# Performance work log

Hardware: AMD Instinct MI355X
Metric: run time of the kernel (lower is better)

Reference implementation:

```python
import jax, jax.numpy as jnp
import numpy as np

HIDDEN, FFN, N_EXPERTS, TOP_K = 1024, 4096, 8, 2


def setup_inputs() -> dict:
    key = jax.random.key(0)
    ks = jax.random.split(key, 8)
    s_h = 1.0 / np.sqrt(HIDDEN)
    s_f = 1.0 / np.sqrt(FFN)
    return {
        "x": jax.random.normal(ks[0], (1, 1024, HIDDEN), dtype=jnp.float32),
        "gate_w": jax.random.normal(ks[1], (N_EXPERTS, HIDDEN), dtype=jnp.float32) * s_h,
        "gate_b": jnp.zeros((N_EXPERTS,), dtype=jnp.float32),
        "w1": jax.random.normal(ks[2], (N_EXPERTS, HIDDEN, FFN), dtype=jnp.float32) * s_h,
        "b1": jnp.zeros((N_EXPERTS, FFN), dtype=jnp.float32),
        "w2": jax.random.normal(ks[3], (N_EXPERTS, FFN, HIDDEN), dtype=jnp.float32) * s_f,
        "b2": jnp.zeros((N_EXPERTS, HIDDEN), dtype=jnp.float32),
    }


def reference(x, gate_w, gate_b, w1, b1, w2, b2):
    B, S, H = x.shape
    x_flat = x.reshape(-1, H)  # (T, H)
    # Router: top-k gating with softmax over selected logits
    logits = x_flat @ gate_w.T + gate_b  # (T, E)
    top_w, sel = jax.lax.top_k(logits, TOP_K)  # (T, K)
    rw = jax.nn.softmax(top_w, axis=-1)  # (T, K)
    # combine[t, e] = router weight of expert e for token t (0 if not selected)
    combine = jnp.sum(jax.nn.one_hot(sel, N_EXPERTS, dtype=x.dtype) * rw[..., None], axis=1)  # (T, E)
    # Dense all-expert FFN, combined with routing weights (zero weight => zero contribution,
    # identical math to the masked gather/scatter loop in the torch module)
    h = jax.nn.gelu(jnp.einsum('th,ehf->tef', x_flat, w1) + b1, approximate=False)  # (T, E, F)
    y = jnp.einsum('tef,efh->teh', h, w2) + b2  # (T, E, H)
    out = jnp.einsum('te,teh->th', combine, y)  # (T, H)
    return out.reshape(B, S, H)
```

## Files before the change

kernel.cpp:

```cpp
#include <hip/hip_runtime.h>


typedef __bf16 bf16;
typedef __bf16 bf16x8 __attribute__((ext_vector_type(8)));
typedef float floatx4 __attribute__((ext_vector_type(4)));

#define T_TOK 1024
#define HID 1024
#define FFN 4096
#define NEXP 8
#define BM 128
#define BN 128
#define BK 32

#define GLOAD16(g, l) __builtin_amdgcn_global_load_lds( \
    (const __attribute__((address_space(1))) void*)(g), \
    (__attribute__((address_space(3))) void*)(l), 16, 0, 0)

__device__ __forceinline__ void wconv_body(const float* __restrict__ w,
                                           bf16* __restrict__ wt, int bid, int tid,
                                           int K, int N, int lgN, int lgKC) {
  int gid = bid * 256 + tid;
  int n = gid & (N - 1);
  int kc = (gid >> lgN) & ((K >> 5) - 1);
  int e = gid >> (lgN + lgKC);
  const float* src = w + ((size_t)e * K + (size_t)kc * 32) * N + n;
  bf16* dst = wt + ((size_t)e * N + n) * (size_t)K + kc * 32;
  float v[32];
#pragma unroll
  for (int j = 0; j < 32; j++) v[j] = src[(size_t)j * N];
  bf16x8 pk[4];
#pragma unroll
  for (int q = 0; q < 4; q++)
#pragma unroll
    for (int i = 0; i < 8; i++) pk[q][i] = (bf16)v[q * 8 + i];
#pragma unroll
  for (int q = 0; q < 4; q++) *(bf16x8*)(dst + q * 8) = pk[q];
}

__device__ __forceinline__ void xconv_body(const float* __restrict__ x,
                                           bf16* __restrict__ xb, int bid, int tid) {
  int i = bid * 256 + tid;
  float4 a = ((const float4*)x)[i * 2];
  float4 b = ((const float4*)x)[i * 2 + 1];
  bf16 t[8] = {(bf16)a.x, (bf16)a.y, (bf16)a.z, (bf16)a.w,
               (bf16)b.x, (bf16)b.y, (bf16)b.z, (bf16)b.w};
  *(bf16x8*)&xb[(size_t)i * 8] = *(bf16x8*)t;
}

__device__ __forceinline__ void router_body(const float* __restrict__ x,
                                            const float* __restrict__ gw,
                                            const float* __restrict__ gb,
                                            int* __restrict__ cnt, int* __restrict__ elist,
                                            float* __restrict__ ewt, int bid, int tid) {
  int wave = tid >> 6;
  int lane = tid & 63;
  int t = bid * 4 + wave;
  const float* xr = x + (size_t)t * HID;
  float xv[16];
#pragma unroll
  for (int j = 0; j < 16; j++) xv[j] = xr[lane + 64 * j];
  float logits[NEXP];
#pragma unroll
  for (int e = 0; e < NEXP; e++) {
    const float* g = gw + (size_t)e * HID;
    float s = 0.f;
#pragma unroll
    for (int j = 0; j < 16; j++) s += xv[j] * g[lane + 64 * j];
#pragma unroll
    for (int off = 32; off; off >>= 1) s += __shfl_xor(s, off, 64);
    logits[e] = s + gb[e];
  }
  int i0 = 0; float l0 = logits[0];
#pragma unroll
  for (int e = 1; e < NEXP; e++) if (logits[e] > l0) { l0 = logits[e]; i0 = e; }
  int i1 = -1; float l1 = -3.0e38f;
#pragma unroll
  for (int e = 0; e < NEXP; e++) if (e != i0 && logits[e] > l1) { l1 = logits[e]; i1 = e; }
  if (lane == 0) {
    float w0 = 1.f / (1.f + expf(l1 - l0));
    float w1 = 1.f - w0;
    int p0 = atomicAdd(cnt + i0, 1);
    elist[i0 * T_TOK + p0] = t * 2 + 0; ewt[i0 * T_TOK + p0] = w0;
    int p1 = atomicAdd(cnt + i1, 1);
    elist[i1 * T_TOK + p1] = t * 2 + 1; ewt[i1 * T_TOK + p1] = w1;
  }
}

__global__ __launch_bounds__(256)
void fusedB_k(const float* __restrict__ x, bf16* __restrict__ xb,
              const float* __restrict__ gw, const float* __restrict__ gb,
              int* __restrict__ cnt, int* __restrict__ elist, float* __restrict__ ewt,
              const float* __restrict__ w1, bf16* __restrict__ w1t) {
  int bid = blockIdx.x;
  int tid = threadIdx.x;
  if (bid < 4096) { wconv_body(w1, w1t, bid, tid, HID, FFN, 12, 5); return; }
  bid -= 4096;
  if (bid < 512) { xconv_body(x, xb, bid, tid); return; }
  router_body(x, gw, gb, cnt, elist, ewt, bid - 512, tid);
}

__global__ __launch_bounds__(256)
void wconv_k(const float* __restrict__ w, bf16* __restrict__ wt,
             int K, int N, int lgN, int lgKC) {
  wconv_body(w, wt, blockIdx.x, threadIdx.x, K, N, lgN, lgKC);
}

__global__ __launch_bounds__(256)
void gemm1f_k(int nconv, const float* __restrict__ w2, bf16* __restrict__ w2t,
              const bf16* __restrict__ xb, const bf16* __restrict__ w1t,
              const float* __restrict__ b1, const int* __restrict__ cnt,
              const int* __restrict__ elist, bf16* __restrict__ hbuf) {
  int tid = threadIdx.x;
  int bid = blockIdx.x;
  if (bid < nconv) { wconv_body(w2, w2t, bid, tid, FFN, HID, 10, 7); return; }
  int g = bid - nconv;
  int e = g >> 8;
  int m0 = ((g >> 5) & 7) * BM;
  int n0 = (g & 31) * BN;
  int c = cnt[e];
  if (m0 >= c) return;

  __shared__ __align__(16) bf16 As[BM][BK];
  __shared__ __align__(16) bf16 Bs[BN][BK];

  int l = tid & 63, w = tid >> 6;
  int rr = w * 32 + (l >> 2);
  int cb = (l & 3) * 8;
  int ga0 = m0 + rr;      if (ga0 >= c) ga0 = c - 1;
  int ga1 = m0 + rr + 16; if (ga1 >= c) ga1 = c - 1;
  const bf16* aS0 = xb + (size_t)(elist[e * T_TOK + ga0] >> 1) * HID + cb;
  const bf16* aS1 = xb + (size_t)(elist[e * T_TOK + ga1] >> 1) * HID + cb;
  const bf16* w1te = w1t + (size_t)e * FFN * HID;
  const bf16* bS0 = w1te + (size_t)(n0 + rr) * HID + cb;
  const bf16* bS1 = w1te + (size_t)(n0 + rr + 16) * HID + cb;
  bf16* ldA0 = &As[w * 32][0];
  bf16* ldA1 = &As[w * 32 + 16][0];
  bf16* ldB0 = &Bs[w * 32][0];
  bf16* ldB1 = &Bs[w * 32 + 16][0];

  floatx4 acc[4][4] = {};
  int fm = l & 15, quad = l >> 4, wm = (w & 1) * 64, wn = (w >> 1) * 64;

  for (int t = 0; t < HID / BK; t++) {
    __syncthreads();
    GLOAD16(aS0, ldA0); GLOAD16(aS1, ldA1);
    GLOAD16(bS0, ldB0); GLOAD16(bS1, ldB1);
    aS0 += BK; aS1 += BK; bS0 += BK; bS1 += BK;
    __syncthreads();
    bf16x8 af[4], bfr[4];
#pragma unroll
    for (int i = 0; i < 4; i++) af[i] = *(const bf16x8*)&As[wm + i * 16 + fm][quad * 8];
#pragma unroll
    for (int j = 0; j < 4; j++) bfr[j] = *(const bf16x8*)&Bs[wn + j * 16 + fm][quad * 8];
#pragma unroll
    for (int i = 0; i < 4; i++)
#pragma unroll
      for (int j = 0; j < 4; j++)
        acc[i][j] = __builtin_amdgcn_mfma_f32_16x16x32_bf16(af[i], bfr[j], acc[i][j], 0, 0, 0);
  }

  const float* b1e = b1 + (size_t)e * FFN;
#pragma unroll
  for (int i = 0; i < 4; i++) {
    int rb = m0 + wm + i * 16 + quad * 4;
#pragma unroll
    for (int j = 0; j < 4; j++) {
      int col = n0 + wn + j * 16 + fm;
      float bias = b1e[col];
#pragma unroll
      for (int r = 0; r < 4; r++) {
        int row = rb + r;
        if (row < c) {
          int slot = elist[e * T_TOK + row];
          float v = acc[i][j][r] + bias;
          float gl = 0.5f * v * (1.f + erff(v * 0.70710678118654752f));
          hbuf[(size_t)slot * FFN + col] = (bf16)gl;
        }
      }
    }
  }
}

__global__ __launch_bounds__(256)
void gemm2_k(const bf16* __restrict__ hbuf, const bf16* __restrict__ w2t,
             const float* __restrict__ b2, const int* __restrict__ cnt,
             const int* __restrict__ elist, const float* __restrict__ ewt,
             float* __restrict__ out) {
  int e = blockIdx.z & 7;
  int ks = blockIdx.z >> 3;
  int c = cnt[e];
  int m0 = blockIdx.y * BM;
  if (m0 >= c) return;
  int n0 = blockIdx.x * BN;
  int kbeg = ks * (FFN / 4);

  __shared__ __align__(16) bf16 As[BM][BK];
  __shared__ __align__(16) bf16 Bs[BN][BK];

  int tid = threadIdx.x;
  int l = tid & 63, w = tid >> 6;
  int rr = w * 32 + (l >> 2);
  int cb = (l & 3) * 8;
  int ga0 = m0 + rr;      if (ga0 >= c) ga0 = c - 1;
  int ga1 = m0 + rr + 16; if (ga1 >= c) ga1 = c - 1;
  const bf16* aS0 = hbuf + (size_t)elist[e * T_TOK + ga0] * FFN + kbeg + cb;
  const bf16* aS1 = hbuf + (size_t)elist[e * T_TOK + ga1] * FFN + kbeg + cb;
  const bf16* w2te = w2t + (size_t)e * HID * FFN;
  const bf16* bS0 = w2te + (size_t)(n0 + rr) * FFN + kbeg + cb;
  const bf16* bS1 = w2te + (size_t)(n0 + rr + 16) * FFN + kbeg + cb;
  bf16* ldA0 = &As[w * 32][0];
  bf16* ldA1 = &As[w * 32 + 16][0];
  bf16* ldB0 = &Bs[w * 32][0];
  bf16* ldB1 = &Bs[w * 32 + 16][0];

  floatx4 acc[4][4] = {};
  int fm = l & 15, quad = l >> 4, wm = (w & 1) * 64, wn = (w >> 1) * 64;

  const int NT = (FFN / 4) / BK;
  for (int t = 0; t < NT; t++) {
    __syncthreads();
    GLOAD16(aS0, ldA0); GLOAD16(aS1, ldA1);
    GLOAD16(bS0, ldB0); GLOAD16(bS1, ldB1);
    aS0 += BK; aS1 += BK; bS0 += BK; bS1 += BK;
    __syncthreads();
    bf16x8 af[4], bfr[4];
#pragma unroll
    for (int i = 0; i < 4; i++) af[i] = *(const bf16x8*)&As[wm + i * 16 + fm][quad * 8];
#pragma unroll
    for (int j = 0; j < 4; j++) bfr[j] = *(const bf16x8*)&Bs[wn + j * 16 + fm][quad * 8];
#pragma unroll
    for (int i = 0; i < 4; i++)
#pragma unroll
      for (int j = 0; j < 4; j++)
        acc[i][j] = __builtin_amdgcn_mfma_f32_16x16x32_bf16(af[i], bfr[j], acc[i][j], 0, 0, 0);
  }

  const float* b2e = b2 + (size_t)e * HID;
#pragma unroll
  for (int i = 0; i < 4; i++) {
    int rb = m0 + wm + i * 16 + quad * 4;
#pragma unroll
    for (int j = 0; j < 4; j++) {
      int col = n0 + wn + j * 16 + fm;
      float bias = (ks == 0) ? b2e[col] : 0.f;
#pragma unroll
      for (int r = 0; r < 4; r++) {
        int row = rb + r;
        if (row < c) {
          int slot = elist[e * T_TOK + row];
          float wgt = ewt[e * T_TOK + row];
          atomicAdd(&out[(size_t)(slot >> 1) * HID + col], wgt * (acc[i][j][r] + bias));
        }
      }
    }
  }
}

extern "C" void kernel_launch(void* const* d_in, const int* in_sizes, int n_in,
                              void* d_out, int out_size, void* d_ws, size_t ws_size,
                              hipStream_t stream) {
  const float* x  = (const float*)d_in[0];
  const float* gw = (const float*)d_in[1];
  const float* gb = (const float*)d_in[2];
  const float* w1 = (const float*)d_in[3];
  const float* b1 = (const float*)d_in[4];
  const float* w2 = (const float*)d_in[5];
  const float* b2 = (const float*)d_in[6];
  float* out = (float*)d_out;

  char* ws = (char*)d_ws;
  int*   cnt   = (int*)ws;
  int*   elist = (int*)(ws + 1024);
  float* ewt   = (float*)(ws + 1024 + 32768);
  bf16*  xb    = (bf16*)(ws + (1 << 16));
  bf16*  hbuf  = (bf16*)(ws + ((size_t)4 << 20));
  bf16*  w1T   = (bf16*)(ws + ((size_t)21 << 20));
  bool par = ws_size >= ((size_t)157 << 20);
  bf16*  w2T   = par ? (bf16*)(ws + ((size_t)89 << 20))
                     : w1T;

  hipMemsetAsync(cnt, 0, 32, stream);
  hipMemsetAsync(out, 0, out_size, stream);
  fusedB_k<<<4864, 256, 0, stream>>>(x, xb, gw, gb, cnt, elist, ewt, w1, w1T);
  if (par) {
    gemm1f_k<<<4096 + 2048, 256, 0, stream>>>(4096, w2, w2T, xb, w1T, b1, cnt, elist, hbuf);
  } else {
    gemm1f_k<<<2048, 256, 0, stream>>>(0, w2, w2T, xb, w1T, b1, cnt, elist, hbuf);
    wconv_k<<<4096, 256, 0, stream>>>(w2, w2T, FFN, HID, 10, 7);
  }
  gemm2_k<<<dim3(HID / BN, T_TOK / BM, NEXP * 4), 256, 0, stream>>>(hbuf, w2T, b2, cnt, elist, ewt, out);
}
```

Baseline: 524.6 us.

## Shrink GEMM M-tile to 64 and deepen K-step to 64 in both expert GEMMs

Both grouped GEMMs now use 64-row by 128-column tiles with a 64-wide K step, stored as two 32-wide LDS halves. Each warp covers all 64 rows and a 32-column strip. In the fused first kernel the GEMM blocks now come first and the w2 conversion blocks come last. Smaller M tiles waste less work on partially filled expert tiles and give more blocks, and the deeper K step halves the number of barriers. The cost is lower reuse per block, since more blocks reload the same weight columns.

```diff
diff --git a/kernel.cpp b/kernel.cpp
--- a/kernel.cpp
+++ b/kernel.cpp
@@ -9,9 +9,9 @@
 #define HID 1024
 #define FFN 4096
 #define NEXP 8
-#define BM 128
+#define BM 64
 #define BN 128
-#define BK 32
+#define BK 64
 
 #define GLOAD16(g, l) __builtin_amdgcn_global_load_lds( \
     (const __attribute__((address_space(1))) void*)(g), \
@@ -107,65 +107,71 @@
 }
 
 __global__ __launch_bounds__(256)
-void gemm1f_k(int nconv, const float* __restrict__ w2, bf16* __restrict__ w2t,
+void gemm1f_k(int ngemm, const float* __restrict__ w2, bf16* __restrict__ w2t,
               const bf16* __restrict__ xb, const bf16* __restrict__ w1t,
               const float* __restrict__ b1, const int* __restrict__ cnt,
               const int* __restrict__ elist, bf16* __restrict__ hbuf) {
   int tid = threadIdx.x;
   int bid = blockIdx.x;
-  if (bid < nconv) { wconv_body(w2, w2t, bid, tid, FFN, HID, 10, 7); return; }
-  int g = bid - nconv;
-  int e = g >> 8;
-  int m0 = ((g >> 5) & 7) * BM;
-  int n0 = (g & 31) * BN;
+  if (bid >= ngemm) { wconv_body(w2, w2t, bid - ngemm, tid, FFN, HID, 10, 7); return; }
+  int e = bid >> 9;
+  int m0 = ((bid >> 5) & 15) * BM;
+  int n0 = (bid & 31) * BN;
   int c = cnt[e];
   if (m0 >= c) return;
 
-  __shared__ __align__(16) bf16 As[BM][BK];
-  __shared__ __align__(16) bf16 Bs[BN][BK];
+  __shared__ __align__(16) bf16 As[2][BM][32];
+  __shared__ __align__(16) bf16 Bs[2][BN][32];
 
   int l = tid & 63, w = tid >> 6;
-  int rr = w * 32 + (l >> 2);
-  int cb = (l & 3) * 8;
-  int ga0 = m0 + rr;      if (ga0 >= c) ga0 = c - 1;
-  int ga1 = m0 + rr + 16; if (ga1 >= c) ga1 = c - 1;
-  const bf16* aS0 = xb + (size_t)(elist[e * T_TOK + ga0] >> 1) * HID + cb;
-  const bf16* aS1 = xb + (size_t)(elist[e * T_TOK + ga1] >> 1) * HID + cb;
+  int l4 = l >> 2;
+  int k8 = (l & 3) * 8;
+  int gra = m0 + w * 16 + l4; if (gra >= c) gra = c - 1;
+  const bf16* ap = xb + (size_t)(elist[e * T_TOK + gra] >> 1) * HID + k8;
   const bf16* w1te = w1t + (size_t)e * FFN * HID;
-  const bf16* bS0 = w1te + (size_t)(n0 + rr) * HID + cb;
-  const bf16* bS1 = w1te + (size_t)(n0 + rr + 16) * HID + cb;
-  bf16* ldA0 = &As[w * 32][0];
-  bf16* ldA1 = &As[w * 32 + 16][0];
-  bf16* ldB0 = &Bs[w * 32][0];
-  bf16* ldB1 = &Bs[w * 32 + 16][0];
-
-  floatx4 acc[4][4] = {};
-  int fm = l & 15, quad = l >> 4, wm = (w & 1) * 64, wn = (w >> 1) * 64;
+  const bf16* bp0 = w1te + (size_t)(n0 + (2 * w) * 16 + l4) * HID + k8;
+  const bf16* bp1 = w1te + (size_t)(n0 + (2 * w + 1) * 16 + l4) * HID + k8;
+  bf16* ldA0 = &As[0][w * 16][0];
+  bf16* ldA1 = &As[1][w * 16][0];
+  bf16* ldB00 = &Bs[0][(2 * w) * 16][0];
+  bf16* ldB01 = &Bs[1][(2 * w) * 16][0];
+  bf16* ldB10 = &Bs[0][(2 * w + 1) * 16][0];
+  bf16* ldB11 = &Bs[1][(2 * w + 1) * 16][0];
+
+  floatx4 acc[4][2] = {};
+  int fm = l & 15, quad = l >> 4;
+  int wn = w * 32;
 
   for (int t = 0; t < HID / BK; t++) {
     __syncthreads();
-    GLOAD16(aS0, ldA0); GLOAD16(aS1, ldA1);
-    GLOAD16(bS0, ldB0); GLOAD16(bS1, ldB1);
-    aS0 += BK; aS1 += BK; bS0 += BK; bS1 += BK;
+    GLOAD16(ap, ldA0);       GLOAD16(ap + 32, ldA1);
+    GLOAD16(bp0, ldB00);     GLOAD16(bp0 + 32, ldB01);
+    GLOAD16(bp1, ldB10);     GLOAD16(bp1 + 32, ldB11);
+    ap += BK; bp0 += BK; bp1 += BK;
     __syncthreads();
-    bf16x8 af[4], bfr[4];
-#pragma unroll
-    for (int i = 0; i < 4; i++) af[i] = *(const bf16x8*)&As[wm + i * 16 + fm][quad * 8];
-#pragma unroll
-    for (int j = 0; j < 4; j++) bfr[j] = *(const bf16x8*)&Bs[wn + j * 16 + fm][quad * 8];
-#pragma unroll
-    for (int i = 0; i < 4; i++)
-#pragma unroll
-      for (int j = 0; j < 4; j++)
-        acc[i][j] = __builtin_amdgcn_mfma_f32_16x16x32_bf16(af[i], bfr[j], acc[i][j], 0, 0, 0);
+    bf16x8 af[2][4], bfr[2][2];
+#pragma unroll
+    for (int kk = 0; kk < 2; kk++) {
+#pragma unroll
+      for (int i = 0; i < 4; i++) af[kk][i] = *(const bf16x8*)&As[kk][i * 16 + fm][quad * 8];
+#pragma unroll
+      for (int j = 0; j < 2; j++) bfr[kk][j] = *(const bf16x8*)&Bs[kk][wn + j * 16 + fm][quad * 8];
+    }
+#pragma unroll
+    for (int kk = 0; kk < 2; kk++)
+#pragma unroll
+      for (int i = 0; i < 4; i++)
+#pragma unroll
+        for (int j = 0; j < 2; j++)
+          acc[i][j] = __builtin_amdgcn_mfma_f32_16x16x32_bf16(af[kk][i], bfr[kk][j], acc[i][j], 0, 0, 0);
   }
 
   const float* b1e = b1 + (size_t)e * FFN;
 #pragma unroll
   for (int i = 0; i < 4; i++) {
-    int rb = m0 + wm + i * 16 + quad * 4;
-#pragma unroll
-    for (int j = 0; j < 4; j++) {
+    int rb = m0 + i * 16 + quad * 4;
+#pragma unroll
+    for (int j = 0; j < 2; j++) {
       int col = n0 + wn + j * 16 + fm;
       float bias = b1e[col];
 #pragma unroll
@@ -195,53 +201,60 @@
   int n0 = blockIdx.x * BN;
   int kbeg = ks * (FFN / 4);
 
-  __shared__ __align__(16) bf16 As[BM][BK];
-  __shared__ __align__(16) bf16 Bs[BN][BK];
+  __shared__ __align__(16) bf16 As[2][BM][32];
+  __shared__ __align__(16) bf16 Bs[2][BN][32];
 
   int tid = threadIdx.x;
   int l = tid & 63, w = tid >> 6;
-  int rr = w * 32 + (l >> 2);
-  int cb = (l & 3) * 8;
-  int ga0 = m0 + rr;      if (ga0 >= c) ga0 = c - 1;
-  int ga1 = m0 + rr + 16; if (ga1 >= c) ga1 = c - 1;
-  const bf16* aS0 = hbuf + (size_t)elist[e * T_TOK + ga0] * FFN + kbeg + cb;
-  const bf16* aS1 = hbuf + (size_t)elist[e * T_TOK + ga1] * FFN + kbeg + cb;
+  int l4 = l >> 2;
+  int k8 = (l & 3) * 8;
+  int gra = m0 + w * 16 + l4; if (gra >= c) gra = c - 1;
+  const bf16* ap = hbuf + (size_t)elist[e * T_TOK + gra] * FFN + kbeg + k8;
   const bf16* w2te = w2t + (size_t)e * HID * FFN;
-  const bf16* bS0 = w2te + (size_t)(n0 + rr) * FFN + kbeg + cb;
-  const bf16* bS1 = w2te + (size_t)(n0 + rr + 16) * FFN + kbeg + cb;
-  bf16* ldA0 = &As[w * 32][0];
-  bf16* ldA1 = &As[w * 32 + 16][0];
-  bf16* ldB0 = &Bs[w * 32][0];
-  bf16* ldB1 = &Bs[w * 32 + 16][0];
-
-  floatx4 acc[4][4] = {};
-  int fm = l & 15, quad = l >> 4, wm = (w & 1) * 64, wn = (w >> 1) * 64;
+  const bf16* bp0 = w2te + (size_t)(n0 + (2 * w) * 16 + l4) * FFN + kbeg + k8;
+  const bf16* bp1 = w2te + (size_t)(n0 + (2 * w + 1) * 16 + l4) * FFN + kbeg + k8;
+  bf16* ldA0 = &As[0][w * 16][0];
+  bf16* ldA1 = &As[1][w * 16][0];
+  bf16* ldB00 = &Bs[0][(2 * w) * 16][0];
+  bf16* ldB01 = &Bs[1][(2 * w) * 16][0];
+  bf16* ldB10 = &Bs[0][(2 * w + 1) * 16][0];
+  bf16* ldB11 = &Bs[1][(2 * w + 1) * 16][0];
+
+  floatx4 acc[4][2] = {};
+  int fm = l & 15, quad = l >> 4;
+  int wn = w * 32;
 
   const int NT = (FFN / 4) / BK;
   for (int t = 0; t < NT; t++) {
     __syncthreads();
-    GLOAD16(aS0, ldA0); GLOAD16(aS1, ldA1);
-    GLOAD16(bS0, ldB0); GLOAD16(bS1, ldB1);
-    aS0 += BK; aS1 += BK; bS0 += BK; bS1 += BK;
+    GLOAD16(ap, ldA0);       GLOAD16(ap + 32, ldA1);
+    GLOAD16(bp0, ldB00);     GLOAD16(bp0 + 32, ldB01);
+    GLOAD16(bp1, ldB10);     GLOAD16(bp1 + 32, ldB11);
+    ap += BK; bp0 += BK; bp1 += BK;
     __syncthreads();
-    bf16x8 af[4], bfr[4];
-#pragma unroll
-    for (int i = 0; i < 4; i++) af[i] = *(const bf16x8*)&As[wm + i * 16 + fm][quad * 8];
-#pragma unroll
-    for (int j = 0; j < 4; j++) bfr[j] = *(const bf16x8*)&Bs[wn + j * 16 + fm][quad * 8];
-#pragma unroll
-    for (int i = 0; i < 4; i++)
-#pragma unroll
-      for (int j = 0; j < 4; j++)
-        acc[i][j] = __builtin_amdgcn_mfma_f32_16x16x32_bf16(af[i], bfr[j], acc[i][j], 0, 0, 0);
+    bf16x8 af[2][4], bfr[2][2];
+#pragma unroll
+    for (int kk = 0; kk < 2; kk++) {
+#pragma unroll
+      for (int i = 0; i < 4; i++) af[kk][i] = *(const bf16x8*)&As[kk][i * 16 + fm][quad * 8];
+#pragma unroll
+      for (int j = 0; j < 2; j++) bfr[kk][j] = *(const bf16x8*)&Bs[kk][wn + j * 16 + fm][quad * 8];
+    }
+#pragma unroll
+    for (int kk = 0; kk < 2; kk++)
+#pragma unroll
+      for (int i = 0; i < 4; i++)
+#pragma unroll
+        for (int j = 0; j < 2; j++)
+          acc[i][j] = __builtin_amdgcn_mfma_f32_16x16x32_bf16(af[kk][i], bfr[kk][j], acc[i][j], 0, 0, 0);
   }
 
   const float* b2e = b2 + (size_t)e * HID;
 #pragma unroll
   for (int i = 0; i < 4; i++) {
-    int rb = m0 + wm + i * 16 + quad * 4;
-#pragma unroll
-    for (int j = 0; j < 4; j++) {
+    int rb = m0 + i * 16 + quad * 4;
+#pragma unroll
+    for (int j = 0; j < 2; j++) {
       int col = n0 + wn + j * 16 + fm;
       float bias = (ks == 0) ? b2e[col] : 0.f;
 #pragma unroll
@@ -284,9 +297,9 @@
   hipMemsetAsync(out, 0, out_size, stream);
   fusedB_k<<<4864, 256, 0, stream>>>(x, xb, gw, gb, cnt, elist, ewt, w1, w1T);
   if (par) {
-    gemm1f_k<<<4096 + 2048, 256, 0, stream>>>(4096, w2, w2T, xb, w1T, b1, cnt, elist, hbuf);
+    gemm1f_k<<<8192, 256, 0, stream>>>(4096, w2, w2T, xb, w1T, b1, cnt, elist, hbuf);
   } else {
-    gemm1f_k<<<2048, 256, 0, stream>>>(0, w2, w2T, xb, w1T, b1, cnt, elist, hbuf);
+    gemm1f_k<<<4096, 256, 0, stream>>>(4096, w2, w2T, xb, w1T, b1, cnt, elist, hbuf);
     wconv_k<<<4096, 256, 0, stream>>>(w2, w2T, FFN, HID, 10, 7);
   }
   gemm2_k<<<dim3(HID / BN, T_TOK / BM, NEXP * 4), 256, 0, stream>>>(hbuf, w2T, b2, cnt, elist, ewt, out);
```

Result: faster. 459.4 us (-12.4%).
